# Kernel optimization log

Measured on AMD Instinct MI355X. Metric: run time of the kernel, lower is better.

Reference implementation:

```python
import jax, jax.numpy as jnp
import numpy as np
from jax.scipy.special import logsumexp

B, S, H, L = 64, 512, 768, 9  # batch, seq_len, bert hidden, num CoNLL labels


def setup_inputs() -> dict:
    key = jax.random.key(0)
    ks = jax.random.split(key, 7)
    hidden = jax.random.normal(ks[0], (B, S, H), jnp.float32)
    cls_w = jax.random.normal(ks[1], (H, L), jnp.float32) * 0.02
    cls_b = jnp.zeros((L,), jnp.float32)
    # pytorch-crf initializes params uniform(-0.1, 0.1)
    start_transitions = jax.random.uniform(ks[2], (L,), jnp.float32, -0.1, 0.1)
    end_transitions = jax.random.uniform(ks[3], (L,), jnp.float32, -0.1, 0.1)
    transitions = jax.random.uniform(ks[4], (L, L), jnp.float32, -0.1, 0.1)
    labels = jax.random.randint(ks[5], (B, S), 0, L).astype(jnp.int64)
    attention_mask = jnp.ones((B, S), jnp.int32)  # CRF requires mask[:, 0] True
    return dict(hidden=hidden, cls_w=cls_w, cls_b=cls_b,
                start_transitions=start_transitions,
                end_transitions=end_transitions, transitions=transitions,
                labels=labels, attention_mask=attention_mask)


def _crf_nll(emissions, tags, mask, start_transitions, end_transitions, transitions):
    # emissions [B,S,L], tags [B,S] int, mask [B,S] bool. pytorch-crf, batch_first.
    maskf = mask.astype(emissions.dtype)
    b = emissions.shape[0]
    # ---- numerator: score of the given tag path ----
    em_tag = jnp.take_along_axis(emissions, tags[..., None], axis=2)[..., 0]  # [B,S]
    trans_score = transitions[tags[:, :-1], tags[:, 1:]]                      # [B,S-1]
    num = (start_transitions[tags[:, 0]] + em_tag[:, 0]
           + jnp.sum((trans_score + em_tag[:, 1:]) * maskf[:, 1:], axis=1))
    seq_ends = jnp.sum(mask, axis=1).astype(jnp.int32) - 1
    last_tags = jnp.take_along_axis(tags, seq_ends[:, None].astype(tags.dtype), axis=1)[:, 0]
    num = num + end_transitions[last_tags]
    # ---- denominator: forward algorithm (log partition) as a scan ----
    def step(score, xs):
        em_t, m_t = xs  # [B,L], [B]
        nxt = logsumexp(score[:, :, None] + transitions[None] + em_t[:, None, :], axis=1)
        return jnp.where(m_t[:, None], nxt, score), None

    init = start_transitions[None, :] + emissions[:, 0]  # [B,L]
    xs = (jnp.swapaxes(emissions[:, 1:], 0, 1), jnp.swapaxes(mask[:, 1:], 0, 1))
    final, _ = jax.lax.scan(step, init, xs)
    denom = logsumexp(final + end_transitions[None, :], axis=1)  # [B]
    llh = num - denom
    return -jnp.mean(llh)  # reduction='mean' over batch, then negated


def reference(hidden, cls_w, cls_b, start_transitions, end_transitions,
              transitions, labels, attention_mask):
    # dropout in eval mode -> identity
    emissions = hidden @ cls_w + cls_b  # [B,S,L]
    mask = attention_mask.astype(bool)
    tags = jnp.where(labels == -100, 0, labels)  # clamp ignored labels to 0
    loss = _crf_nll(emissions, tags, mask, start_transitions,
                    end_transitions, transitions)
    return (loss, emissions)
```

## Files before the change

kernel.cpp:

```cpp
#include <hip/hip_runtime.h>

#define BB 64
#define SS 512
#define HH 768
#define LL 9
#define NROWS (BB * SS)
#define NCHUNK 16
#define CLEN 32

#define L2E 1.4426950408889634f
#define LN2 0.6931471805599453f
#define NEGINF (-1e30f)

__global__ __launch_bounds__(256, 2) void emis_gemm(
    const float* __restrict__ hidden, const float* __restrict__ w,
    const float* __restrict__ bias, float* __restrict__ emis) {
  __shared__ float part[8][65][12];
  const int tid = threadIdx.x;
  const int lane = tid & 63;
  const int wv = tid >> 6;

  float W[3][4][LL];
#pragma unroll
  for (int kk = 0; kk < 3; ++kk) {
    const int kbase = lane * 4 + 256 * kk;
#pragma unroll
    for (int e = 0; e < 4; ++e)
#pragma unroll
      for (int j = 0; j < LL; ++j)
        W[kk][e][j] = w[(kbase + e) * LL + j];
  }
  const int rr = tid / 9, jj = tid - rr * 9;
  const float bj = (tid < 72) ? bias[jj] : 0.f;

  const int r0 = wv * 2, r1 = r0 + 1;
  for (int g = blockIdx.x; g < NROWS / 8; g += gridDim.x) {
    const int rowbase = g * 8;
    const float4* hA = reinterpret_cast<const float4*>(hidden + (size_t)(rowbase + r0) * HH);
    const float4* hB = reinterpret_cast<const float4*>(hidden + (size_t)(rowbase + r1) * HH);
    const float4 a0 = hA[lane], a1 = hA[lane + 64], a2 = hA[lane + 128];
    const float4 b0 = hB[lane], b1 = hB[lane + 64], b2 = hB[lane + 128];
    float acc0[LL], acc1[LL];
#pragma unroll
    for (int j = 0; j < LL; ++j) {
      acc0[j] = a0.x * W[0][0][j] + a0.y * W[0][1][j] + a0.z * W[0][2][j] + a0.w * W[0][3][j]
              + a1.x * W[1][0][j] + a1.y * W[1][1][j] + a1.z * W[1][2][j] + a1.w * W[1][3][j]
              + a2.x * W[2][0][j] + a2.y * W[2][1][j] + a2.z * W[2][2][j] + a2.w * W[2][3][j];
      acc1[j] = b0.x * W[0][0][j] + b0.y * W[0][1][j] + b0.z * W[0][2][j] + b0.w * W[0][3][j]
              + b1.x * W[1][0][j] + b1.y * W[1][1][j] + b1.z * W[1][2][j] + b1.w * W[1][3][j]
              + b2.x * W[2][0][j] + b2.y * W[2][1][j] + b2.z * W[2][2][j] + b2.w * W[2][3][j];
    }
    float4* p0 = reinterpret_cast<float4*>(&part[r0][lane][0]);
    p0[0] = make_float4(acc0[0], acc0[1], acc0[2], acc0[3]);
    p0[1] = make_float4(acc0[4], acc0[5], acc0[6], acc0[7]);
    part[r0][lane][8] = acc0[8];
    float4* p1 = reinterpret_cast<float4*>(&part[r1][lane][0]);
    p1[0] = make_float4(acc1[0], acc1[1], acc1[2], acc1[3]);
    p1[1] = make_float4(acc1[4], acc1[5], acc1[6], acc1[7]);
    part[r1][lane][8] = acc1[8];
    __syncthreads();
    if (tid < 72) {
      float s0 = 0.f, s1 = 0.f, s2 = 0.f, s3 = 0.f;
#pragma unroll
      for (int l = 0; l < 64; l += 4) {
        s0 += part[rr][l + 0][jj];
        s1 += part[rr][l + 1][jj];
        s2 += part[rr][l + 2][jj];
        s3 += part[rr][l + 3][jj];
      }
      emis[(size_t)(rowbase + rr) * LL + jj] = (s0 + s1) + (s2 + s3) + bj;
    }
    __syncthreads();
  }
}

__global__ __launch_bounds__(128) void crf_chunk(
    const float* __restrict__ emis, const int* __restrict__ msk,
    const float* __restrict__ startT, const float* __restrict__ trans,
    float* __restrict__ initv, float* __restrict__ Pmat) {
  __shared__ float em_lds[CLEN * LL];
  __shared__ int mk_lds[CLEN];
  const int b = blockIdx.x >> 4;
  const int c = blockIdx.x & 15;
  const int tid = threadIdx.x;
  const int lane = tid & 63;
  const int wid = tid >> 6;

  const float* src = emis + ((size_t)b * SS + c * CLEN) * LL;
  for (int i = tid; i < CLEN * LL; i += 128) em_lds[i] = src[i];
  for (int i = tid; i < CLEN; i += 128) mk_lds[i] = msk[b * SS + c * CLEN + i];
  __syncthreads();

  int rloc = lane / 9;
  int j = lane - rloc * 9;
  if (rloc > 6) { rloc = 6; j = 8; }
  const int rbase = rloc * 9;
  const bool active = (wid == 0) ? (lane < 63) : (lane < 18);
  const int r = wid * 7 + rloc;

  float Tc[LL];
#pragma unroll
  for (int i = 0; i < LL; ++i) Tc[i] = trans[i * LL + j];

  float s;
  if (c == 0) s = startT[j] + em_lds[j];
  else s = (j == r) ? 0.f : NEGINF;
  const int t0 = (c == 0) ? 1 : 0;

  for (int t = t0; t < CLEN; ++t) {
    const float emj = em_lds[t * LL + j];
    const int mt = mk_lds[t];
    const float s0 = __shfl(s, rbase + 0), s1 = __shfl(s, rbase + 1), s2 = __shfl(s, rbase + 2);
    const float s3 = __shfl(s, rbase + 3), s4 = __shfl(s, rbase + 4), s5 = __shfl(s, rbase + 5);
    const float s6 = __shfl(s, rbase + 6), s7 = __shfl(s, rbase + 7), s8 = __shfl(s, rbase + 8);
    const float a0 = s0 + Tc[0], a1 = s1 + Tc[1], a2 = s2 + Tc[2];
    const float a3 = s3 + Tc[3], a4 = s4 + Tc[4], a5 = s5 + Tc[5];
    const float a6 = s6 + Tc[6], a7 = s7 + Tc[7], a8 = s8 + Tc[8];
    const float m = fmaxf(fmaxf(fmaxf(fmaxf(a0, a1), fmaxf(a2, a3)),
                                fmaxf(fmaxf(a4, a5), fmaxf(a6, a7))), a8);
    const float e =
        ((exp2f((a0 - m) * L2E) + exp2f((a1 - m) * L2E)) +
         (exp2f((a2 - m) * L2E) + exp2f((a3 - m) * L2E))) +
        ((exp2f((a4 - m) * L2E) + exp2f((a5 - m) * L2E)) +
         (exp2f((a6 - m) * L2E) + exp2f((a7 - m) * L2E))) +
        exp2f((a8 - m) * L2E);
    const float snew = m + LN2 * log2f(e) + emj;
    s = mt ? snew : s;
  }

  if (active) {
    if (c == 0) {
      if (wid == 0 && lane < LL) initv[b * LL + j] = s;
    } else {
      Pmat[((size_t)b * NCHUNK + c) * 81 + r * LL + j] = s;
    }
  }
}

__global__ __launch_bounds__(64) void crf_combine(
    const float* __restrict__ emis, const int* __restrict__ labels,
    const int* __restrict__ msk, const float* __restrict__ startT,
    const float* __restrict__ endT, const float* __restrict__ trans,
    const float* __restrict__ initv, const float* __restrict__ Pmat,
    float* __restrict__ llh) {
  __shared__ float Pl[15 * 81];
  const int b = blockIdx.x;
  const int lane = threadIdx.x;
  const float* __restrict__ emb = emis + (size_t)b * SS * LL;
  const int* __restrict__ lab = labels + b * SS;
  const int* __restrict__ mk = msk + b * SS;

  const float* Pb = Pmat + (size_t)b * NCHUNK * 81 + 81;
  for (int i = lane; i < 15 * 81; i += 64) Pl[i] = Pb[i];

  float acc = 0.f;
  int msum = 0;
  for (int t = lane; t < SS; t += 64) {
    int tg = lab[t]; if (tg == -100) tg = 0;
    const int mt = mk[t];
    msum += mt;
    if (t == 0) {
      acc += startT[tg] + emb[tg];
    } else {
      int tp = lab[t - 1]; if (tp == -100) tp = 0;
      acc += (trans[tp * LL + tg] + emb[t * LL + tg]) * (float)mt;
    }
  }
#pragma unroll
  for (int off = 32; off; off >>= 1) {
    acc += __shfl_xor(acc, off);
    msum += __shfl_xor(msum, off);
  }
  const int seq_end = msum - 1;
  int lt = lab[seq_end]; if (lt == -100) lt = 0;
  const float num = acc + endT[lt];

  __syncthreads();

  const int j = (lane < LL) ? lane : 8;
  float a = initv[b * LL + j];
#pragma unroll 1
  for (int c = 0; c < 15; ++c) {
    const float* P = &Pl[c * 81];
    const float s0 = __shfl(a, 0), s1 = __shfl(a, 1), s2 = __shfl(a, 2);
    const float s3 = __shfl(a, 3), s4 = __shfl(a, 4), s5 = __shfl(a, 5);
    const float s6 = __shfl(a, 6), s7 = __shfl(a, 7), s8 = __shfl(a, 8);
    const float a0 = s0 + P[0 * LL + j], a1 = s1 + P[1 * LL + j], a2 = s2 + P[2 * LL + j];
    const float a3 = s3 + P[3 * LL + j], a4 = s4 + P[4 * LL + j], a5 = s5 + P[5 * LL + j];
    const float a6 = s6 + P[6 * LL + j], a7 = s7 + P[7 * LL + j], a8 = s8 + P[8 * LL + j];
    const float m = fmaxf(fmaxf(fmaxf(fmaxf(a0, a1), fmaxf(a2, a3)),
                                fmaxf(fmaxf(a4, a5), fmaxf(a6, a7))), a8);
    const float e =
        ((exp2f((a0 - m) * L2E) + exp2f((a1 - m) * L2E)) +
         (exp2f((a2 - m) * L2E) + exp2f((a3 - m) * L2E))) +
        ((exp2f((a4 - m) * L2E) + exp2f((a5 - m) * L2E)) +
         (exp2f((a6 - m) * L2E) + exp2f((a7 - m) * L2E))) +
        exp2f((a8 - m) * L2E);
    a = m + LN2 * log2f(e);
  }
  a += endT[j];
  {
    const float s0 = __shfl(a, 0), s1 = __shfl(a, 1), s2 = __shfl(a, 2);
    const float s3 = __shfl(a, 3), s4 = __shfl(a, 4), s5 = __shfl(a, 5);
    const float s6 = __shfl(a, 6), s7 = __shfl(a, 7), s8 = __shfl(a, 8);
    const float m = fmaxf(fmaxf(fmaxf(fmaxf(s0, s1), fmaxf(s2, s3)),
                                fmaxf(fmaxf(s4, s5), fmaxf(s6, s7))), s8);
    const float e =
        ((exp2f((s0 - m) * L2E) + exp2f((s1 - m) * L2E)) +
         (exp2f((s2 - m) * L2E) + exp2f((s3 - m) * L2E))) +
        ((exp2f((s4 - m) * L2E) + exp2f((s5 - m) * L2E)) +
         (exp2f((s6 - m) * L2E) + exp2f((s7 - m) * L2E))) +
        exp2f((s8 - m) * L2E);
    const float denom = m + LN2 * log2f(e);
    if (lane == 0) llh[b] = num - denom;
  }
}

__global__ __launch_bounds__(64) void finalize(const float* __restrict__ llh,
                                               float* __restrict__ out) {
  float v = llh[threadIdx.x];
#pragma unroll
  for (int off = 32; off; off >>= 1) v += __shfl_xor(v, off);
  if (threadIdx.x == 0) out[0] = -v * (1.0f / BB);
}

extern "C" void kernel_launch(void* const* d_in, const int* in_sizes, int n_in,
                              void* d_out, int out_size, void* d_ws, size_t ws_size,
                              hipStream_t stream) {
  const float* hidden = (const float*)d_in[0];
  const float* cls_w  = (const float*)d_in[1];
  const float* cls_b  = (const float*)d_in[2];
  const float* startT = (const float*)d_in[3];
  const float* endT   = (const float*)d_in[4];
  const float* trans  = (const float*)d_in[5];
  const int* labels   = (const int*)d_in[6];
  const int* amask    = (const int*)d_in[7];

  float* out = (float*)d_out;
  float* emis = out + 1;

  float* llh = (float*)d_ws;
  float* initv = llh + 64;
  float* Pmat = initv + 64 * LL;

  emis_gemm<<<1024, 256, 0, stream>>>(hidden, cls_w, cls_b, emis);
  crf_chunk<<<BB * NCHUNK, 128, 0, stream>>>(emis, amask, startT, trans, initv, Pmat);
  crf_combine<<<BB, 64, 0, stream>>>(emis, labels, amask, startT, endT, trans, initv, Pmat, llh);
  finalize<<<1, 64, 0, stream>>>(llh, out);
}
```

Measured before the change: 197.9 us.

## Compute emission GEMM with one thread per row instead of cross-lane reduction

Replaces the block-cooperative emission GEMM, which held the weights in registers, split K across lanes and reduced partial sums through LDS, with a kernel where each thread owns a whole hidden row. Each thread streams that row as float4 and reads the weights as wave-uniform loads. This removes the LDS reduction and both barriers. In exchange, lanes in a wave now read addresses 3 KB apart, so hidden-state loads are no longer coalesced and each thread walks a long serial K loop. That could hurt memory efficiency on the 100 MB input.

```diff
diff --git a/kernel.cpp b/kernel.cpp
--- a/kernel.cpp
+++ b/kernel.cpp
@@ -12,66 +12,35 @@
 #define LN2 0.6931471805599453f
 #define NEGINF (-1e30f)
 
-__global__ __launch_bounds__(256, 2) void emis_gemm(
+__global__ __launch_bounds__(128) void emis_gemm(
     const float* __restrict__ hidden, const float* __restrict__ w,
     const float* __restrict__ bias, float* __restrict__ emis) {
-  __shared__ float part[8][65][12];
-  const int tid = threadIdx.x;
-  const int lane = tid & 63;
-  const int wv = tid >> 6;
-
-  float W[3][4][LL];
-#pragma unroll
-  for (int kk = 0; kk < 3; ++kk) {
-    const int kbase = lane * 4 + 256 * kk;
-#pragma unroll
-    for (int e = 0; e < 4; ++e)
+  const int row = blockIdx.x * 128 + threadIdx.x;
+  const float4* __restrict__ hp =
+      reinterpret_cast<const float4*>(hidden + (size_t)row * HH);
+
+  float acc[LL];
+#pragma unroll
+  for (int j = 0; j < LL; ++j) acc[j] = 0.f;
+
+#pragma unroll 2
+  for (int kb = 0; kb < 24; ++kb) {
+    float4 h[8];
+#pragma unroll
+    for (int u = 0; u < 8; ++u) h[u] = hp[kb * 8 + u];
+    const float* __restrict__ wb = w + kb * 8 * 4 * LL;
+#pragma unroll
+    for (int u = 0; u < 8; ++u) {
+      const float* __restrict__ wq = wb + u * 4 * LL;
 #pragma unroll
       for (int j = 0; j < LL; ++j)
-        W[kk][e][j] = w[(kbase + e) * LL + j];
-  }
-  const int rr = tid / 9, jj = tid - rr * 9;
-  const float bj = (tid < 72) ? bias[jj] : 0.f;
-
-  const int r0 = wv * 2, r1 = r0 + 1;
-  for (int g = blockIdx.x; g < NROWS / 8; g += gridDim.x) {
-    const int rowbase = g * 8;
-    const float4* hA = reinterpret_cast<const float4*>(hidden + (size_t)(rowbase + r0) * HH);
-    const float4* hB = reinterpret_cast<const float4*>(hidden + (size_t)(rowbase + r1) * HH);
-    const float4 a0 = hA[lane], a1 = hA[lane + 64], a2 = hA[lane + 128];
-    const float4 b0 = hB[lane], b1 = hB[lane + 64], b2 = hB[lane + 128];
-    float acc0[LL], acc1[LL];
-#pragma unroll
-    for (int j = 0; j < LL; ++j) {
-      acc0[j] = a0.x * W[0][0][j] + a0.y * W[0][1][j] + a0.z * W[0][2][j] + a0.w * W[0][3][j]
-              + a1.x * W[1][0][j] + a1.y * W[1][1][j] + a1.z * W[1][2][j] + a1.w * W[1][3][j]
-              + a2.x * W[2][0][j] + a2.y * W[2][1][j] + a2.z * W[2][2][j] + a2.w * W[2][3][j];
-      acc1[j] = b0.x * W[0][0][j] + b0.y * W[0][1][j] + b0.z * W[0][2][j] + b0.w * W[0][3][j]
-              + b1.x * W[1][0][j] + b1.y * W[1][1][j] + b1.z * W[1][2][j] + b1.w * W[1][3][j]
-              + b2.x * W[2][0][j] + b2.y * W[2][1][j] + b2.z * W[2][2][j] + b2.w * W[2][3][j];
+        acc[j] += h[u].x * wq[j] + h[u].y * wq[j + LL] +
+                  h[u].z * wq[j + 2 * LL] + h[u].w * wq[j + 3 * LL];
     }
-    float4* p0 = reinterpret_cast<float4*>(&part[r0][lane][0]);
-    p0[0] = make_float4(acc0[0], acc0[1], acc0[2], acc0[3]);
-    p0[1] = make_float4(acc0[4], acc0[5], acc0[6], acc0[7]);
-    part[r0][lane][8] = acc0[8];
-    float4* p1 = reinterpret_cast<float4*>(&part[r1][lane][0]);
-    p1[0] = make_float4(acc1[0], acc1[1], acc1[2], acc1[3]);
-    p1[1] = make_float4(acc1[4], acc1[5], acc1[6], acc1[7]);
-    part[r1][lane][8] = acc1[8];
-    __syncthreads();
-    if (tid < 72) {
-      float s0 = 0.f, s1 = 0.f, s2 = 0.f, s3 = 0.f;
-#pragma unroll
-      for (int l = 0; l < 64; l += 4) {
-        s0 += part[rr][l + 0][jj];
-        s1 += part[rr][l + 1][jj];
-        s2 += part[rr][l + 2][jj];
-        s3 += part[rr][l + 3][jj];
-      }
-      emis[(size_t)(rowbase + rr) * LL + jj] = (s0 + s1) + (s2 + s3) + bj;
-    }
-    __syncthreads();
-  }
+  }
+#pragma unroll
+  for (int j = 0; j < LL; ++j)
+    emis[(size_t)row * LL + j] = acc[j] + bias[j];
 }
 
 __global__ __launch_bounds__(128) void crf_chunk(
@@ -243,7 +212,7 @@
   float* initv = llh + 64;
   float* Pmat = initv + 64 * LL;
 
-  emis_gemm<<<1024, 256, 0, stream>>>(hidden, cls_w, cls_b, emis);
+  emis_gemm<<<NROWS / 128, 128, 0, stream>>>(hidden, cls_w, cls_b, emis);
   crf_chunk<<<BB * NCHUNK, 128, 0, stream>>>(emis, amask, startT, trans, initv, Pmat);
   crf_combine<<<BB, 64, 0, stream>>>(emis, labels, amask, startT, endT, trans, initv, Pmat, llh);
   finalize<<<1, 64, 0, stream>>>(llh, out);
```

After: 322.2 us. 1.63x slower.
